# Performance work log

Hardware: AMD Instinct MI355X
Metric: run time of the kernel (lower is better)

The kernel has to match this reference:

```python
import jax, jax.numpy as jnp
import numpy as np

B, S, HID = 2, 2048, 2048
NH, NKV, HD = 16, 4, 128
GROUPS = NH // NKV
CLIP = 8.0
ROPE_THETA = 500000.0
QKV_OUT = HID + 2 * NKV * HD  # 3072
NEG = jnp.finfo(jnp.float32).min


def setup_inputs() -> dict:
    key = jax.random.key(0)
    k1, k2, k3 = jax.random.split(key, 3)
    hidden_states = jax.random.normal(k1, (B, S, HID), dtype=jnp.float32)
    position_ids = jnp.tile(jnp.arange(S, dtype=jnp.int64)[None, :], (B, 1))
    Wqkv = jax.random.normal(k2, (QKV_OUT, HID), dtype=jnp.float32) * (HID ** -0.5)
    Wout = jax.random.normal(k3, (HID, HID), dtype=jnp.float32) * (HID ** -0.5)
    return {"hidden_states": hidden_states, "position_ids": position_ids,
            "Wqkv": Wqkv, "Wout": Wout}


def _rotate_half(x):
    x1, x2 = jnp.split(x, 2, axis=-1)
    return jnp.concatenate((-x2, x1), axis=-1)


def reference(hidden_states, position_ids, Wqkv, Wout):
    b, s, _ = hidden_states.shape
    # fused QKV projection + clamp
    qkv = jnp.einsum('bsh,oh->bso', hidden_states, Wqkv)
    qkv = jnp.clip(qkv, -CLIP, CLIP)
    q, k, v = jnp.split(qkv, [HID, HID + NKV * HD], axis=2)
    q = q.reshape(b, s, NH, HD).transpose(0, 2, 1, 3)   # [b, nh, s, hd]
    k = k.reshape(b, s, NKV, HD).transpose(0, 2, 1, 3)  # [b, nkv, s, hd]
    v = v.reshape(b, s, NKV, HD).transpose(0, 2, 1, 3)
    # rotary embedding
    inv_freq = 1.0 / (ROPE_THETA ** (jnp.arange(0, HD, 2, dtype=jnp.float32) / HD))
    freqs = position_ids.astype(jnp.float32)[:, :, None] * inv_freq[None, None, :]  # [b,s,hd/2]
    emb = jnp.concatenate((freqs, freqs), axis=-1)      # [b, s, hd]
    cos = jnp.cos(emb)[:, None, :, :]                   # [b, 1, s, hd]
    sin = jnp.sin(emb)[:, None, :, :]
    q = q * cos + _rotate_half(q) * sin
    k = k * cos + _rotate_half(k) * sin
    # repeat kv heads (GQA)
    k = jnp.repeat(k, GROUPS, axis=1)  # [b, nh, s, hd]
    v = jnp.repeat(v, GROUPS, axis=1)
    # attention with additive causal mask
    scores = jnp.einsum('bhqd,bhkd->bhqk', q, k) / jnp.sqrt(jnp.float32(HD))
    causal = jnp.where(jnp.tril(jnp.ones((s, s), dtype=bool)), 0.0, NEG)
    scores = scores + causal[None, None, :, :]
    attn = jax.nn.softmax(scores.astype(jnp.float32), axis=-1).astype(q.dtype)
    out = jnp.einsum('bhqk,bhkd->bhqd', attn, v)
    out = out.transpose(0, 2, 1, 3).reshape(b, s, HID)
    return jnp.einsum('bsh,oh->bso', out, Wout)
```

## Files before the change

kernel.cpp:

```cpp
#include <hip/hip_runtime.h>
#include <stdint.h>

#define S_    2048
#define HID_  2048
#define NH_   16
#define NKV_  4
#define HD_   128

using short4x = __attribute__((ext_vector_type(4))) short;
using short8  = __attribute__((ext_vector_type(8))) short;
using floatx4 = __attribute__((ext_vector_type(4))) float;

#define NEGBIG (-3.0e38f)

__device__ __forceinline__ unsigned short f2bf(float x) {
  union { float f; unsigned u; } v; v.f = x;
  unsigned r = v.u + 0x7fffu + ((v.u >> 16) & 1u);
  return (unsigned short)(r >> 16);
}
__device__ __forceinline__ float bf2f(unsigned short b) {
  union { unsigned u; float f; } v; v.u = ((unsigned)b) << 16;
  return v.f;
}
__device__ __forceinline__ void ld_lds16(const void* g, void* l) {
  __builtin_amdgcn_global_load_lds(
      (const __attribute__((address_space(1))) unsigned*)g,
      (__attribute__((address_space(3))) unsigned*)l, 16, 0, 0);
}

__global__ void k_cvt(const float* __restrict__ src, unsigned short* __restrict__ dst, int n4) {
  int i = blockIdx.x * blockDim.x + threadIdx.x;
  if (i >= n4) return;
  float4 v = ((const float4*)src)[i];
  union { unsigned short us[4]; uint2 u2; } u;
  u.us[0] = f2bf(v.x); u.us[1] = f2bf(v.y); u.us[2] = f2bf(v.z); u.us[3] = f2bf(v.w);
  ((uint2*)dst)[i] = u.u2;
}

__global__ void k_rope(unsigned short* __restrict__ buf, const int* __restrict__ pos,
                       int nh, float oscale) {
  unsigned idx = blockIdx.x * blockDim.x + threadIdx.x;
  int d = idx & 63;
  int h = (idx >> 6) % nh;
  int m = idx / (unsigned)(nh << 6);
  float p = (float)pos[m];
  float inv = expf(-(float)d * (13.122363377404328f / 64.0f));
  float f = p * inv;
  float cs = cosf(f), sn = sinf(f);
  size_t base = (size_t)m * (nh * HD_) + h * HD_ + d;
  float x1 = bf2f(buf[base]), x2 = bf2f(buf[base + 64]);
  buf[base]      = f2bf((x1 * cs - x2 * sn) * oscale);
  buf[base + 64] = f2bf((x2 * cs + x1 * sn) * oscale);
}

template <int EPI>
__global__ void __launch_bounds__(256)
k_gemm_bt(const unsigned short* __restrict__ A, const unsigned short* __restrict__ Bw,
          unsigned short* __restrict__ Qb, unsigned short* __restrict__ Kb,
          unsigned short* __restrict__ Vt, float* __restrict__ Of) {
  const int K = HID_;
  __shared__ __align__(16) unsigned short As[128 * 32];
  __shared__ __align__(16) unsigned short Bs[128 * 32];
  const int tid  = threadIdx.x;
  const int wave = tid >> 6, lane = tid & 63;
  const int quad = lane >> 4, l15 = lane & 15;
  const int wm = (wave >> 1) * 64, wn = (wave & 1) * 64;
  const int m0 = blockIdx.x * 128, n0 = blockIdx.y * 128;

  floatx4 acc[4][4] = {};

  const int srow = tid >> 2;
  const int scol = (tid & 3) * 8;
  const unsigned short* Ag0 = A  + (size_t)(m0 + srow)      * K + scol;
  const unsigned short* Ag1 = A  + (size_t)(m0 + 64 + srow) * K + scol;
  const unsigned short* Bg0 = Bw + (size_t)(n0 + srow)      * K + scol;
  const unsigned short* Bg1 = Bw + (size_t)(n0 + 64 + srow) * K + scol;
  unsigned short* lA0 = &As[tid * 8];
  unsigned short* lA1 = &As[2048 + tid * 8];
  unsigned short* lB0 = &Bs[tid * 8];
  unsigned short* lB1 = &Bs[2048 + tid * 8];

  for (int k0 = 0; k0 < K; k0 += 32) {
    __syncthreads();
    ld_lds16(Ag0 + k0, lA0);
    ld_lds16(Ag1 + k0, lA1);
    ld_lds16(Bg0 + k0, lB0);
    ld_lds16(Bg1 + k0, lB1);
    __syncthreads();
    short8 a[4], b[4];
#pragma unroll
    for (int i = 0; i < 4; i++) a[i] = *(const short8*)&As[(wm + i * 16 + l15) * 32 + quad * 8];
#pragma unroll
    for (int j = 0; j < 4; j++) b[j] = *(const short8*)&Bs[(wn + j * 16 + l15) * 32 + quad * 8];
#pragma unroll
    for (int i = 0; i < 4; i++)
#pragma unroll
      for (int j = 0; j < 4; j++)
        acc[i][j] = __builtin_amdgcn_mfma_f32_16x16x32_bf16(a[i], b[j], acc[i][j], 0, 0, 0);
  }

#pragma unroll
  for (int i = 0; i < 4; i++) {
#pragma unroll
    for (int j = 0; j < 4; j++) {
      const int col = n0 + wn + j * 16 + l15;
#pragma unroll
      for (int r = 0; r < 4; r++) {
        const int row = m0 + wm + i * 16 + quad * 4 + r;
        float x = acc[i][j][r];
        if (EPI == 0) {
          x = fminf(fmaxf(x, -8.0f), 8.0f);
          if (col < HID_) {
            Qb[(size_t)row * HID_ + col] = f2bf(x);
          } else if (col < HID_ + NKV_ * HD_) {
            Kb[(size_t)row * (NKV_ * HD_) + (col - HID_)] = f2bf(x);
          } else {
            int oo = col - (HID_ + NKV_ * HD_);
            int kvh = oo >> 7, d = oo & 127;
            int bb = row >> 11, ss = row & 2047;
            Vt[((size_t)((bb * NKV_ + kvh) * HD_ + d) << 11) + ss] = f2bf(x);
          }
        } else {
          Of[(size_t)row * HID_ + col] = x;
        }
      }
    }
  }
}

__global__ void __launch_bounds__(256, 2)
k_attn(const unsigned short* __restrict__ Qb, const unsigned short* __restrict__ Kb,
       const unsigned short* __restrict__ Vt, unsigned short* __restrict__ AO) {
  __shared__ __align__(16) unsigned short sm[2][16384];
  __shared__ __align__(16) unsigned short Pl[4][16][80];

  const int tid  = threadIdx.x;
  const int wave = tid >> 6, lane = tid & 63;
  const int quad = lane >> 4, l15 = lane & 15;
  const int tLow  = blockIdx.x;
  const int tHigh = 31 - tLow;
  const int q0L = tLow * 64, q0H = tHigh * 64;
  const int bh = blockIdx.y;
  const int b = bh >> 4, h = bh & 15;
  const int kvh = h >> 2;

  const int srow = tid >> 2;
  const int scol = (tid & 3) * 8;

  {
    const unsigned short* qgL = Qb + (size_t)(b * S_ + q0L + srow) * HID_ + h * HD_ + scol;
    const unsigned short* qgH = Qb + (size_t)(b * S_ + q0H + srow) * HID_ + h * HD_ + scol;
#pragma unroll
    for (int i = 0; i < 4; i++) ld_lds16(qgL + i * 32, &sm[0][i * 2048 + tid * 8]);
#pragma unroll
    for (int i = 0; i < 4; i++) ld_lds16(qgH + i * 32, &sm[1][i * 2048 + tid * 8]);
  }
  __syncthreads();
  short8 qaL[4], qaH[4];
#pragma unroll
  for (int c = 0; c < 4; c++) {
    qaL[c] = *(const short8*)&sm[0][(c * 64 + wave * 16 + l15) * 32 + quad * 8];
    qaH[c] = *(const short8*)&sm[1][(c * 64 + wave * 16 + l15) * 32 + quad * 8];
  }
  __syncthreads();

  floatx4 oacL[8] = {}, oacH[8] = {};
  floatx4 oacEL = {}, oacEH = {};
  float mL = NEGBIG, mH = NEGBIG;

  const unsigned short* kgb = Kb + (size_t)b * S_ * (NKV_ * HD_) + kvh * HD_ + scol;
  const unsigned short* vgb = Vt + (size_t)(b * NKV_ + kvh) * HD_ * S_;

  unsigned short* PlW = &Pl[wave][0][0];

  short8 ones;
#pragma unroll
  for (int i = 0; i < 8; i++) ones[i] = (short)0x3F80;

  auto stage = [&](int bufI, int j) {
    unsigned short* B = &sm[bufI][0];
    const unsigned short* kg = kgb + (size_t)(j * 64 + srow) * (NKV_ * HD_);
#pragma unroll
    for (int i = 0; i < 4; i++) ld_lds16(kg + i * 32, &B[i * 2048 + tid * 8]);
#pragma unroll
    for (int i = 0; i < 4; i++) {
      int c = i >> 1, rowd = (i & 1) * 64 + srow;
      ld_lds16(vgb + (size_t)rowd * S_ + j * 64 + c * 32 + scol,
               &B[8192 + c * 4096 + (i & 1) * 2048 + tid * 8]);
    }
  };

  auto attn_step = [&](const short8* qa, floatx4* oac, floatx4& oacE, float& m_run,
                       int q0, int j, bool diag, const unsigned short* Kt,
                       const unsigned short* Vts) {
    floatx4 sc[4] = {};
#pragma unroll
    for (int t = 0; t < 4; t++)
#pragma unroll
      for (int c = 0; c < 4; c++) {
        short8 ka = *(const short8*)&Kt[c * 2048 + (t * 16 + l15) * 32 + quad * 8];
        sc[t] = __builtin_amdgcn_mfma_f32_16x16x32_bf16(ka, qa[c], sc[t], 0, 0, 0);
      }

    if (diag) {
      const int rowq = q0 + wave * 16 + l15;
#pragma unroll
      for (int t = 0; t < 4; t++) {
        const int kb0 = j * 64 + t * 16 + quad * 4;
#pragma unroll
        for (int r = 0; r < 4; r++)
          if (kb0 + r > rowq) sc[t][r] = NEGBIG;
      }
    }

    float mx = sc[0][0];
#pragma unroll
    for (int t = 0; t < 4; t++)
#pragma unroll
      for (int r = 0; r < 4; r++) mx = fmaxf(mx, sc[t][r]);
    mx = fmaxf(mx, __shfl_xor(mx, 16));
    mx = fmaxf(mx, __shfl_xor(mx, 32));

    const float mo = m_run;
    m_run = fmaxf(mo, mx);
    if (__any(mx > mo)) {
      float alpha = __builtin_amdgcn_exp2f(mo - m_run);
      float al4[4];
#pragma unroll
      for (int r = 0; r < 4; r++) al4[r] = __shfl(alpha, quad * 4 + r, 16);
#pragma unroll
      for (int t = 0; t < 8; t++)
#pragma unroll
        for (int r = 0; r < 4; r++) oac[t][r] *= al4[r];
#pragma unroll
      for (int r = 0; r < 4; r++) oacE[r] *= al4[r];
    }

#pragma unroll
    for (int t = 0; t < 4; t++) {
      short4x pk;
#pragma unroll
      for (int r = 0; r < 4; r++)
        pk[r] = (short)f2bf(__builtin_amdgcn_exp2f(sc[t][r] - m_run));
      *(short4x*)&PlW[l15 * 80 + t * 16 + quad * 4] = pk;
    }

    short8 pa0 = *(const short8*)&PlW[l15 * 80 + quad * 8];
    short8 pa1 = *(const short8*)&PlW[l15 * 80 + 32 + quad * 8];
#pragma unroll
    for (int t = 0; t < 8; t++) {
      short8 vb0 = *(const short8*)&Vts[(t * 16 + l15) * 32 + quad * 8];
      oac[t] = __builtin_amdgcn_mfma_f32_16x16x32_bf16(pa0, vb0, oac[t], 0, 0, 0);
      short8 vb1 = *(const short8*)&Vts[4096 + (t * 16 + l15) * 32 + quad * 8];
      oac[t] = __builtin_amdgcn_mfma_f32_16x16x32_bf16(pa1, vb1, oac[t], 0, 0, 0);
    }
    oacE = __builtin_amdgcn_mfma_f32_16x16x32_bf16(pa0, ones, oacE, 0, 0, 0);
    oacE = __builtin_amdgcn_mfma_f32_16x16x32_bf16(pa1, ones, oacE, 0, 0, 0);
  };

  stage(0, 0);
  int cur = 0;
  for (int j = 0; j <= tHigh; ++j) {
    __syncthreads();
    if (j < tHigh) stage(cur ^ 1, j + 1);
    const unsigned short* Kt  = &sm[cur][0];
    const unsigned short* Vts = Kt + 8192;
    attn_step(qaH, oacH, oacEH, mH, q0H, j, j == tHigh, Kt, Vts);
    if (j <= tLow) attn_step(qaL, oacL, oacEL, mL, q0L, j, j == tLow, Kt, Vts);
    cur ^= 1;
  }

#pragma unroll
  for (int t = 0; t < 8; t++)
#pragma unroll
    for (int r = 0; r < 4; r++) {
      int rgL = q0L + wave * 16 + quad * 4 + r;
      int rgH = q0H + wave * 16 + quad * 4 + r;
      AO[(size_t)(b * S_ + rgL) * HID_ + h * HD_ + t * 16 + l15] = f2bf(oacL[t][r] / oacEL[r]);
      AO[(size_t)(b * S_ + rgH) * HID_ + h * HD_ + t * 16 + l15] = f2bf(oacH[t][r] / oacEH[r]);
    }
}

extern "C" void kernel_launch(void* const* d_in, const int* in_sizes, int n_in,
                              void* d_out, int out_size, void* d_ws, size_t ws_size,
                              hipStream_t stream) {
  (void)in_sizes; (void)n_in; (void)out_size; (void)ws_size;
  const float* hidden = (const float*)d_in[0];
  const int*   pos    = (const int*)d_in[1];
  const float* Wqkv   = (const float*)d_in[2];
  const float* Wout   = (const float*)d_in[3];
  float* out = (float*)d_out;

  unsigned short* ws = (unsigned short*)d_ws;
  const size_t M1 = 1024 * 1024;
  unsigned short* hb  = ws;
  unsigned short* wqb = ws + 8 * M1;
  unsigned short* wob = ws + 14 * M1;
  unsigned short* Qb  = ws + 18 * M1;
  unsigned short* Kb  = ws + 26 * M1;
  unsigned short* Vt  = ws + 28 * M1;
  unsigned short* AO  = hb;

  const float QSCL = 0.08838834764831845f * 1.4426950408889634f;

  k_cvt<<<8192, 256, 0, stream>>>(hidden, hb, 2097152);
  k_cvt<<<6144, 256, 0, stream>>>(Wqkv, wqb, 1572864);
  k_cvt<<<4096, 256, 0, stream>>>(Wout, wob, 1048576);
  k_gemm_bt<0><<<dim3(32, 24), 256, 0, stream>>>(hb, wqb, Qb, Kb, Vt, nullptr);
  k_rope<<<16384, 256, 0, stream>>>(Qb, pos, NH_, QSCL);
  k_rope<<<4096, 256, 0, stream>>>(Kb, pos, NKV_, 1.0f);
  k_attn<<<dim3(16, 32), 256, 0, stream>>>(Qb, Kb, Vt, AO);
  k_gemm_bt<1><<<dim3(32, 16), 256, 0, stream>>>(AO, wob, nullptr, nullptr, nullptr, out);
}
```

Measured before the change: 324.0 us.

## Double-buffer GEMM LDS tiles and merge convert and rope launches

The GEMM now uses two LDS buffers, issuing global-to-LDS loads for the next K slice before computing on the current one, with one barrier per iteration instead of two. The three fp32-to-bf16 conversion kernels are merged into one launch, as are the Q and K rope kernels. This is meant to hide global load latency in the projections and remove launch gaps. In exchange the GEMM uses twice the LDS, which may lower occupancy. There is also a possible race: the async LDS loads may not have finished when the single barrier is reached.

Measured after the change: 329.3 us. About the same (+1.6%).

```diff
diff --git a/kernel.cpp b/kernel.cpp
--- a/kernel.cpp
+++ b/kernel.cpp
@@ -28,18 +28,26 @@
       (__attribute__((address_space(3))) unsigned*)l, 16, 0, 0);
 }
 
-__global__ void k_cvt(const float* __restrict__ src, unsigned short* __restrict__ dst, int n4) {
+__global__ void k_cvt3(const float* __restrict__ s0, unsigned short* __restrict__ d0, int n0,
+                       const float* __restrict__ s1, unsigned short* __restrict__ d1, int n1,
+                       const float* __restrict__ s2, unsigned short* __restrict__ d2, int n2) {
   int i = blockIdx.x * blockDim.x + threadIdx.x;
-  if (i >= n4) return;
-  float4 v = ((const float4*)src)[i];
+  const float* s; unsigned short* d;
+  if (i < n0) { s = s0; d = d0; }
+  else if (i < n0 + n1) { s = s1; d = d1; i -= n0; }
+  else { s = s2; d = d2; i -= n0 + n1; if (i >= n2) return; }
+  float4 v = ((const float4*)s)[i];
   union { unsigned short us[4]; uint2 u2; } u;
   u.us[0] = f2bf(v.x); u.us[1] = f2bf(v.y); u.us[2] = f2bf(v.z); u.us[3] = f2bf(v.w);
-  ((uint2*)dst)[i] = u.u2;
-}
-
-__global__ void k_rope(unsigned short* __restrict__ buf, const int* __restrict__ pos,
-                       int nh, float oscale) {
-  unsigned idx = blockIdx.x * blockDim.x + threadIdx.x;
+  ((uint2*)d)[i] = u.u2;
+}
+
+__global__ void k_rope2(unsigned short* __restrict__ Qb, unsigned short* __restrict__ Kb,
+                        const int* __restrict__ pos, int nQ, float qscale) {
+  int idx = blockIdx.x * blockDim.x + threadIdx.x;
+  unsigned short* buf; int nh; float oscale;
+  if (idx < nQ) { buf = Qb; nh = NH_; oscale = qscale; }
+  else { buf = Kb; nh = NKV_; oscale = 1.0f; idx -= nQ; }
   int d = idx & 63;
   int h = (idx >> 6) % nh;
   int m = idx / (unsigned)(nh << 6);
@@ -59,8 +67,8 @@
           unsigned short* __restrict__ Qb, unsigned short* __restrict__ Kb,
           unsigned short* __restrict__ Vt, float* __restrict__ Of) {
   const int K = HID_;
-  __shared__ __align__(16) unsigned short As[128 * 32];
-  __shared__ __align__(16) unsigned short Bs[128 * 32];
+  __shared__ __align__(16) unsigned short As[2][128 * 32];
+  __shared__ __align__(16) unsigned short Bs[2][128 * 32];
   const int tid  = threadIdx.x;
   const int wave = tid >> 6, lane = tid & 63;
   const int quad = lane >> 4, l15 = lane & 15;
@@ -75,28 +83,30 @@
   const unsigned short* Ag1 = A  + (size_t)(m0 + 64 + srow) * K + scol;
   const unsigned short* Bg0 = Bw + (size_t)(n0 + srow)      * K + scol;
   const unsigned short* Bg1 = Bw + (size_t)(n0 + 64 + srow) * K + scol;
-  unsigned short* lA0 = &As[tid * 8];
-  unsigned short* lA1 = &As[2048 + tid * 8];
-  unsigned short* lB0 = &Bs[tid * 8];
-  unsigned short* lB1 = &Bs[2048 + tid * 8];
-
+
+  auto stage = [&](int buf, int k0) {
+    ld_lds16(Ag0 + k0, &As[buf][tid * 8]);
+    ld_lds16(Ag1 + k0, &As[buf][2048 + tid * 8]);
+    ld_lds16(Bg0 + k0, &Bs[buf][tid * 8]);
+    ld_lds16(Bg1 + k0, &Bs[buf][2048 + tid * 8]);
+  };
+
+  stage(0, 0);
+  int cur = 0;
   for (int k0 = 0; k0 < K; k0 += 32) {
     __syncthreads();
-    ld_lds16(Ag0 + k0, lA0);
-    ld_lds16(Ag1 + k0, lA1);
-    ld_lds16(Bg0 + k0, lB0);
-    ld_lds16(Bg1 + k0, lB1);
-    __syncthreads();
+    if (k0 + 32 < K) stage(cur ^ 1, k0 + 32);
     short8 a[4], b[4];
 #pragma unroll
-    for (int i = 0; i < 4; i++) a[i] = *(const short8*)&As[(wm + i * 16 + l15) * 32 + quad * 8];
-#pragma unroll
-    for (int j = 0; j < 4; j++) b[j] = *(const short8*)&Bs[(wn + j * 16 + l15) * 32 + quad * 8];
+    for (int i = 0; i < 4; i++) a[i] = *(const short8*)&As[cur][(wm + i * 16 + l15) * 32 + quad * 8];
+#pragma unroll
+    for (int j = 0; j < 4; j++) b[j] = *(const short8*)&Bs[cur][(wn + j * 16 + l15) * 32 + quad * 8];
 #pragma unroll
     for (int i = 0; i < 4; i++)
 #pragma unroll
       for (int j = 0; j < 4; j++)
         acc[i][j] = __builtin_amdgcn_mfma_f32_16x16x32_bf16(a[i], b[j], acc[i][j], 0, 0, 0);
+    cur ^= 1;
   }
 
 #pragma unroll
@@ -302,13 +312,14 @@
   unsigned short* AO  = hb;
 
   const float QSCL = 0.08838834764831845f * 1.4426950408889634f;
-
-  k_cvt<<<8192, 256, 0, stream>>>(hidden, hb, 2097152);
-  k_cvt<<<6144, 256, 0, stream>>>(Wqkv, wqb, 1572864);
-  k_cvt<<<4096, 256, 0, stream>>>(Wout, wob, 1048576);
+  const int nQrope = 2 * 2048 * NH_ * 64;
+  const int nKrope = 2 * 2048 * NKV_ * 64;
+
+  k_cvt3<<<18432, 256, 0, stream>>>(hidden, hb, 2097152,
+                                    Wqkv, wqb, 1572864,
+                                    Wout, wob, 1048576);
   k_gemm_bt<0><<<dim3(32, 24), 256, 0, stream>>>(hb, wqb, Qb, Kb, Vt, nullptr);
-  k_rope<<<16384, 256, 0, stream>>>(Qb, pos, NH_, QSCL);
-  k_rope<<<4096, 256, 0, stream>>>(Kb, pos, NKV_, 1.0f);
+  k_rope2<<<(nQrope + nKrope) / 256, 256, 0, stream>>>(Qb, Kb, pos, nQrope, QSCL);
   k_attn<<<dim3(16, 32), 256, 0, stream>>>(Qb, Kb, Vt, AO);
   k_gemm_bt<1><<<dim3(32, 16), 256, 0, stream>>>(AO, wob, nullptr, nullptr, nullptr, out);
 }
```
